# Optimization experiments

Hardware: AMD Instinct MI355X
Metric: run time of the kernel (lower is better)

The kernel has to match this reference:

```python
import jax, jax.numpy as jnp
import numpy as np

B, H, W, C = 16, 64, 64, 256
C8 = C // 8

def setup_inputs() -> dict:
    key = jax.random.key(0)
    ks = jax.random.split(key, 8)
    return {
        "x": jax.random.normal(ks[0], (B, H, W, C), dtype=jnp.float32),
        "Wf": jax.random.normal(ks[1], (C, C8), dtype=jnp.float32) * 0.05,
        "Wg": jax.random.normal(ks[2], (C, C8), dtype=jnp.float32) * 0.05,
        "Wh": jax.random.normal(ks[3], (C, C), dtype=jnp.float32) * 0.05,
        "bf": jax.random.normal(ks[4], (C8,), dtype=jnp.float32) * 0.05,
        "bg": jax.random.normal(ks[5], (C8,), dtype=jnp.float32) * 0.05,
        "bh": jax.random.normal(ks[6], (C,), dtype=jnp.float32) * 0.05,
        "gamma": jax.random.normal(ks[7], (1,), dtype=jnp.float32) * 0.05,
    }

def reference(x, Wf, Wg, Wh, bf, bg, bh, gamma):
    # 1x1 convs == per-pixel channel matmuls (NHWC)
    f = jnp.einsum('bhwc,cd->bhwd', x, Wf) + bf  # [B,H,W,C/8]
    g = jnp.einsum('bhwc,cd->bhwd', x, Wg) + bg  # [B,H,W,C/8]
    h = jnp.einsum('bhwc,cd->bhwd', x, Wh) + bh  # [B,H,W,C]
    b = x.shape[0]
    # K.batch_flatten flattens all non-batch dims -> attention over BATCH dim
    gf = g.reshape(b, -1)                      # [B, HWC/8]
    ff = f.reshape(b, -1)                      # [B, HWC/8]
    hf = h.reshape(b, -1)                      # [B, HWC]
    s = gf @ ff.T                              # [B, B]
    beta = jax.nn.softmax(s, axis=-1)          # softmax over batch axis
    o = (beta @ hf).reshape(x.shape)           # [B,H,W,C]
    # activation=None -> linear; gamma-scaled residual
    return gamma * o + x
```

## Files before the change

### kernel.cpp

```cpp
#include <hip/hip_runtime.h>

typedef __attribute__((ext_vector_type(4))) float  f4;
typedef __attribute__((ext_vector_type(2))) float  f2;
typedef __attribute__((ext_vector_type(8))) short  short8;
typedef __attribute__((ext_vector_type(4))) float  f32x4;
typedef __attribute__((ext_vector_type(2))) unsigned int u32x2;

static __device__ __forceinline__ unsigned short f2bf(float f) {
    unsigned u = __builtin_bit_cast(unsigned, f);
    unsigned r = (u + 0x7FFFu + ((u >> 16) & 1u)) >> 16;
    return (unsigned short)r;
}
static __device__ __forceinline__ float bf2f(unsigned short h) {
    return __builtin_bit_cast(float, ((unsigned)h) << 16);
}

__global__ __launch_bounds__(256) void k_setup(const float* __restrict__ Wh,
                                               const float* __restrict__ bh,
                                               const float* __restrict__ Wf,
                                               const float* __restrict__ Wg,
                                               const float* __restrict__ gamma,
                                               unsigned short* __restrict__ WhT,
                                               float* __restrict__ gb,
                                               unsigned short* __restrict__ Wfg_hi,
                                               unsigned short* __restrict__ Wfg_lo) {
    __shared__ float T[8 * 260];
    const int t = threadIdx.x, b = blockIdx.x;
    const float g = gamma[0];
    if (b < 32) {
        const int c0 = b * 8;
        const int cr = t >> 5, q = t & 31;
        f4 v0 = *(const f4*)(Wh + (c0 + cr) * 256 + q * 8);
        f4 v1 = *(const f4*)(Wh + (c0 + cr) * 256 + q * 8 + 4);
        *(f4*)(T + cr * 260 + q * 8)     = v0;
        *(f4*)(T + cr * 260 + q * 8 + 4) = v1;
        __syncthreads();
        short8 o;
        #pragma unroll
        for (int j = 0; j < 8; ++j) o[j] = (short)f2bf(g * T[j * 260 + t]);
        *(short8*)(WhT + t * 256 + c0) = o;
    } else {
        gb[t] = g * bh[t];
        const int n = t >> 2, cq = t & 3;
        const float* Wsrc = (n < 32) ? Wf : Wg;
        const int nn = n & 31;
        #pragma unroll
        for (int c8 = 0; c8 < 8; ++c8) {
            short8 h8, l8;
            #pragma unroll
            for (int k = 0; k < 8; ++k) {
                const int c = cq * 64 + c8 * 8 + k;
                const float v = Wsrc[c * 32 + nn];
                const unsigned short h = f2bf(v);
                h8[k] = (short)h;
                l8[k] = (short)f2bf(v - bf2f(h));
            }
            *(short8*)(Wfg_hi + n * 256 + cq * 64 + c8 * 8) = h8;
            *(short8*)(Wfg_lo + n * 256 + cq * 64 + c8 * 8) = l8;
        }
    }
}

__global__ __launch_bounds__(256, 2) void ka(const float* __restrict__ x,
                                             const unsigned short* __restrict__ Wfg_hi,
                                             const unsigned short* __restrict__ Wfg_lo,
                                             const float* __restrict__ bfv,
                                             const float* __restrict__ bgv,
                                             float* __restrict__ s_part) {
    __shared__ __align__(16) unsigned char smem[65536];

    const int t = threadIdx.x, w = t >> 6, l = t & 63;
    const int p = blockIdx.x * 4 + w;

    f4 xr[16];
    #pragma unroll
    for (int j = 0; j < 16; ++j)
        xr[j] = *(const f4*)(x + (((j << 12) + p) << 8) + l * 4);
    #pragma unroll
    for (int j = 0; j < 16; ++j) {
        const int r = j * 4 + w;
        int bo = r * 512 + l * 8;
        bo ^= (r & 7) << 4;
        const unsigned short h0 = f2bf(xr[j][0]), h1 = f2bf(xr[j][1]);
        const unsigned short h2 = f2bf(xr[j][2]), h3 = f2bf(xr[j][3]);
        u32x2 ph, pl;
        ph[0] = ((unsigned)h1 << 16) | h0;
        ph[1] = ((unsigned)h3 << 16) | h2;
        const unsigned short e0 = f2bf(xr[j][0] - bf2f(h0));
        const unsigned short e1 = f2bf(xr[j][1] - bf2f(h1));
        const unsigned short e2 = f2bf(xr[j][2] - bf2f(h2));
        const unsigned short e3 = f2bf(xr[j][3] - bf2f(h3));
        pl[0] = ((unsigned)e1 << 16) | e0;
        pl[1] = ((unsigned)e3 << 16) | e2;
        *(u32x2*)(smem + bo)         = ph;
        *(u32x2*)(smem + 32768 + bo) = pl;
    }
    __syncthreads();

    const int lrow = l & 15;
    const int kfe  = (l >> 4) * 8;
    const int ncol = w * 16 + lrow;
    f32x4 acc[4];
    #pragma unroll
    for (int mt = 0; mt < 4; ++mt) acc[mt] = (f32x4){0.f, 0.f, 0.f, 0.f};

    #pragma unroll
    for (int k0 = 0; k0 < 256; k0 += 32) {
        const short8 bh_ = *(const short8*)(Wfg_hi + ncol * 256 + k0 + kfe);
        const short8 bl_ = *(const short8*)(Wfg_lo + ncol * 256 + k0 + kfe);
        short8 ah[4], al[4];
        #pragma unroll
        for (int mt = 0; mt < 4; ++mt) {
            const int row = mt * 16 + lrow;
            int bo = row * 512 + (k0 + kfe) * 2;
            bo ^= (row & 7) << 4;
            ah[mt] = *(const short8*)(smem + bo);
            al[mt] = *(const short8*)(smem + 32768 + bo);
        }
        #pragma unroll
        for (int mt = 0; mt < 4; ++mt) {
            acc[mt] = __builtin_amdgcn_mfma_f32_16x16x32_bf16(ah[mt], bh_, acc[mt], 0, 0, 0);
            acc[mt] = __builtin_amdgcn_mfma_f32_16x16x32_bf16(al[mt], bh_, acc[mt], 0, 0, 0);
            acc[mt] = __builtin_amdgcn_mfma_f32_16x16x32_bf16(ah[mt], bl_, acc[mt], 0, 0, 0);
        }
    }
    __syncthreads();

    float* FG = (float*)smem;
    const float bias = (ncol < 32) ? bfv[ncol] : bgv[ncol - 32];
    #pragma unroll
    for (int mt = 0; mt < 4; ++mt)
        #pragma unroll
        for (int jj = 0; jj < 4; ++jj) {
            const int row = mt * 16 + (l >> 4) * 4 + jj;
            FG[row * 68 + ncol] = acc[mt][jj] + bias;
        }
    __syncthreads();

    const int si = t >> 4, sj = t & 15;
    float sacc = 0.f;
    #pragma unroll
    for (int q = 0; q < 4; ++q) {
        const float* Gp = FG + (si * 4 + q) * 68 + 32;
        const float* Fp = FG + (sj * 4 + q) * 68;
        #pragma unroll
        for (int d4 = 0; d4 < 8; ++d4) {
            f4 gv = *(const f4*)(Gp + d4 * 4);
            f4 fv = *(const f4*)(Fp + d4 * 4);
            sacc += gv[0] * fv[0] + gv[1] * fv[1] + gv[2] * fv[2] + gv[3] * fv[3];
        }
    }
    s_part[blockIdx.x * 256 + si * 16 + sj] = sacc;
}

__global__ __launch_bounds__(256) void kb1(const float* __restrict__ s_part,
                                           float* __restrict__ s_red) {
    const int t = threadIdx.x, b = blockIdx.x;
    float a = 0.f;
    #pragma unroll
    for (int k = 0; k < 16; ++k) a += s_part[(b * 16 + k) * 256 + t];
    s_red[b * 256 + t] = a;
}

__global__ __launch_bounds__(1024) void kb2(const float* __restrict__ s_red,
                                            float* __restrict__ beta) {
    __shared__ float red[4 * 256];
    __shared__ float srow[256];
    __shared__ float erow[256];
    const int t = threadIdx.x;
    const int pair = t & 255;
    const int qr = t >> 8;
    float a = 0.f;
    #pragma unroll
    for (int b = qr * 16; b < qr * 16 + 16; ++b) a += s_red[b * 256 + pair];
    red[qr * 256 + pair] = a;
    __syncthreads();
    float s = 0.f, e = 0.f;
    if (t < 256) {
        s = red[pair] + red[256 + pair] + red[512 + pair] + red[768 + pair];
        srow[pair] = s;
    }
    __syncthreads();
    if (t < 256) {
        const int i = pair >> 4;
        float m = srow[i * 16];
        #pragma unroll
        for (int j = 1; j < 16; ++j) m = fmaxf(m, srow[i * 16 + j]);
        e = expf(s - m);
        erow[pair] = e;
    }
    __syncthreads();
    if (t < 256) {
        const int i = pair >> 4;
        float sum = 0.f;
        #pragma unroll
        for (int j = 0; j < 16; ++j) sum += erow[i * 16 + j];
        beta[pair] = e / sum;
    }
}

__global__ __launch_bounds__(256, 3) void kc(const float* __restrict__ x,
                                             const unsigned short* __restrict__ WhT,
                                             const float* __restrict__ gb,
                                             const float* __restrict__ beta,
                                             float* __restrict__ out) {
    __shared__ __align__(16) unsigned char smem[34048];
    float* beta_l = (float*)(smem + 33024);

    const int t = threadIdx.x;
    const int w = t >> 6;
    const int l = t & 63;
    const int p0 = blockIdx.x * 4;
    const int p  = p0 + w;
    const int cbase = l * 4;

    f4 xr[16];
    #pragma unroll
    for (int j = 0; j < 16; ++j)
        xr[j] = *(const f4*)(x + (((j << 12) + p) << 8) + cbase);
    if (t < 64) *(f4*)(beta_l + t * 4) = *(const f4*)(beta + t * 4);
    __syncthreads();

    #pragma unroll
    for (int i = 0; i < 16; ++i) {
        f4 bv0 = *(const f4*)(beta_l + i * 16);
        f4 bv1 = *(const f4*)(beta_l + i * 16 + 4);
        f4 bv2 = *(const f4*)(beta_l + i * 16 + 8);
        f4 bv3 = *(const f4*)(beta_l + i * 16 + 12);
        f4 a = {0.f, 0.f, 0.f, 0.f};
        #pragma unroll
        for (int j = 0; j < 4; ++j) {
            a += xr[j]      * bv0[j];
            a += xr[4 + j]  * bv1[j];
            a += xr[8 + j]  * bv2[j];
            a += xr[12 + j] * bv3[j];
        }
        const int r = i * 4 + w;
        int bo = r * 512 + l * 8;
        bo ^= (r & 7) << 4;
        u32x2 packed;
        packed[0] = ((unsigned)f2bf(a[1]) << 16) | f2bf(a[0]);
        packed[1] = ((unsigned)f2bf(a[3]) << 16) | f2bf(a[2]);
        *(u32x2*)(smem + bo) = packed;
    }
    __syncthreads();

    f32x4 acc[4][4];
    #pragma unroll
    for (int mt = 0; mt < 4; ++mt)
        #pragma unroll
        for (int nt = 0; nt < 4; ++nt) acc[mt][nt] = (f32x4){0.f, 0.f, 0.f, 0.f};

    const int n0 = w * 64;
    const int lrow = l & 15;
    const int hi = l >> 4;
    const int kf = hi * 8;
    const unsigned short* wbase = WhT + (n0 + lrow) * 256 + kf;

    short8 bcur[4], bnxt[4];
    #pragma unroll
    for (int nt = 0; nt < 4; ++nt)
        bcur[nt] = *(const short8*)(wbase + nt * 16 * 256);

    #pragma unroll
    for (int ks = 0; ks < 8; ++ks) {
        const int k0 = ks * 32;
        if (ks < 7) {
            #pragma unroll
            for (int nt = 0; nt < 4; ++nt)
                bnxt[nt] = *(const short8*)(wbase + nt * 16 * 256 + k0 + 32);
        }
        short8 af[4];
        #pragma unroll
        for (int mt = 0; mt < 4; ++mt) {
            const int row = mt * 16 + lrow;
            int bo = row * 512 + (k0 + kf) * 2;
            bo ^= (row & 7) << 4;
            af[mt] = *(const short8*)(smem + bo);
        }
        #pragma unroll
        for (int mt = 0; mt < 4; ++mt)
            #pragma unroll
            for (int nt = 0; nt < 4; ++nt)
                acc[mt][nt] = __builtin_amdgcn_mfma_f32_16x16x32_bf16(
                    af[mt], bcur[nt], acc[mt][nt], 0, 0, 0);
        #pragma unroll
        for (int nt = 0; nt < 4; ++nt) bcur[nt] = bnxt[nt];
    }

    float* cst = (float*)smem;
    const f4 gb4 = *(const f4*)(gb + cbase);
    #pragma unroll
    for (int h = 0; h < 2; ++h) {
        __syncthreads();
        #pragma unroll
        for (int mt2 = 0; mt2 < 2; ++mt2) {
            const int mt = h * 2 + mt2;
            #pragma unroll
            for (int nt = 0; nt < 4; ++nt)
                #pragma unroll
                for (int j = 0; j < 4; ++j) {
                    const int rl = mt2 * 16 + hi * 4 + j;
                    cst[rl * 258 + n0 + nt * 16 + lrow] = acc[mt][nt][j];
                }
        }
        __syncthreads();
        #pragma unroll
        for (int rr = 0; rr < 8; ++rr) {
            const int rl = rr * 4 + w;
            const int rg = h * 32 + rl;
            const int i  = rg >> 2, q = rg & 3;
            const int idx = (((i << 12) + p0 + q) << 8) + cbase;
            f4 o = *(const f4*)(cst + rl * 258 + cbase);
            o += gb4 + *(const f4*)(x + idx);
            __builtin_nontemporal_store(o, (f4*)(out + idx));
        }
    }
}

extern "C" void kernel_launch(void* const* d_in, const int* in_sizes, int n_in,
                              void* d_out, int out_size, void* d_ws, size_t ws_size,
                              hipStream_t stream) {
    const float* x     = (const float*)d_in[0];
    const float* Wf    = (const float*)d_in[1];
    const float* Wg    = (const float*)d_in[2];
    const float* Wh    = (const float*)d_in[3];
    const float* bfv   = (const float*)d_in[4];
    const float* bgv   = (const float*)d_in[5];
    const float* bhv   = (const float*)d_in[6];
    const float* gamma = (const float*)d_in[7];
    float* out = (float*)d_out;

    char* ws = (char*)d_ws;
    unsigned short* WhT = (unsigned short*)ws;
    float* gb     = (float*)(ws + 131072);
    float* beta   = (float*)(ws + 132096);
    float* s_part = (float*)(ws + 133120);
    unsigned short* Wfg_hi = (unsigned short*)(ws + 1181696);
    unsigned short* Wfg_lo = (unsigned short*)(ws + 1214464);
    float* s_red  = (float*)(ws + 1181696);

    k_setup<<<dim3(33), dim3(256), 0, stream>>>(Wh, bhv, Wf, Wg, gamma, WhT, gb, Wfg_hi, Wfg_lo);
    ka<<<dim3(1024), dim3(256), 0, stream>>>(x, Wfg_hi, Wfg_lo, bfv, bgv, s_part);
    kb1<<<dim3(64), dim3(256), 0, stream>>>(s_part, s_red);
    kb2<<<dim3(1), dim3(1024), 0, stream>>>(s_red, beta);
    kc<<<dim3(1024), dim3(256), 0, stream>>>(x, WhT, gb, beta, out);
}
```

Before: 79.81 us.

## Process two pixel groups per block in kc, prefetching second x tile

Each kc block now handles two groups of four pixels instead of one, and the grid is halved. The second group's x rows are loaded into registers while the first group is being mixed and multiplied, so global load latency overlaps with MFMA and epilogue work. The staging and output shared-memory buffers are split so the second mix does not have to wait for the first epilogue's buffer. The cost is much higher register and LDS use, with launch bounds lowered to 2 blocks per CU, which reduces occupancy.

Result: no change. 80.07 us (+0.3%).

```diff
diff --git a/kernel.cpp b/kernel.cpp
--- a/kernel.cpp
+++ b/kernel.cpp
@@ -199,28 +199,8 @@
     }
 }
 
-__global__ __launch_bounds__(256, 3) void kc(const float* __restrict__ x,
-                                             const unsigned short* __restrict__ WhT,
-                                             const float* __restrict__ gb,
-                                             const float* __restrict__ beta,
-                                             float* __restrict__ out) {
-    __shared__ __align__(16) unsigned char smem[34048];
-    float* beta_l = (float*)(smem + 33024);
-
-    const int t = threadIdx.x;
-    const int w = t >> 6;
-    const int l = t & 63;
-    const int p0 = blockIdx.x * 4;
-    const int p  = p0 + w;
-    const int cbase = l * 4;
-
-    f4 xr[16];
-    #pragma unroll
-    for (int j = 0; j < 16; ++j)
-        xr[j] = *(const f4*)(x + (((j << 12) + p) << 8) + cbase);
-    if (t < 64) *(f4*)(beta_l + t * 4) = *(const f4*)(beta + t * 4);
-    __syncthreads();
-
+__device__ __forceinline__ void kc_mix(const f4 (&xr)[16], const float* beta_l,
+                                       unsigned char* stage, int w, int l) {
     #pragma unroll
     for (int i = 0; i < 16; ++i) {
         f4 bv0 = *(const f4*)(beta_l + i * 16);
@@ -241,21 +221,16 @@
         u32x2 packed;
         packed[0] = ((unsigned)f2bf(a[1]) << 16) | f2bf(a[0]);
         packed[1] = ((unsigned)f2bf(a[3]) << 16) | f2bf(a[2]);
-        *(u32x2*)(smem + bo) = packed;
-    }
-    __syncthreads();
-
-    f32x4 acc[4][4];
+        *(u32x2*)(stage + bo) = packed;
+    }
+}
+
+__device__ __forceinline__ void kc_gemm(f32x4 (&acc)[4][4], const unsigned char* stage,
+                                        const unsigned short* wbase, int lrow, int kf) {
     #pragma unroll
     for (int mt = 0; mt < 4; ++mt)
         #pragma unroll
         for (int nt = 0; nt < 4; ++nt) acc[mt][nt] = (f32x4){0.f, 0.f, 0.f, 0.f};
-
-    const int n0 = w * 64;
-    const int lrow = l & 15;
-    const int hi = l >> 4;
-    const int kf = hi * 8;
-    const unsigned short* wbase = WhT + (n0 + lrow) * 256 + kf;
 
     short8 bcur[4], bnxt[4];
     #pragma unroll
@@ -276,7 +251,7 @@
             const int row = mt * 16 + lrow;
             int bo = row * 512 + (k0 + kf) * 2;
             bo ^= (row & 7) << 4;
-            af[mt] = *(const short8*)(smem + bo);
+            af[mt] = *(const short8*)(stage + bo);
         }
         #pragma unroll
         for (int mt = 0; mt < 4; ++mt)
@@ -287,9 +262,12 @@
         #pragma unroll
         for (int nt = 0; nt < 4; ++nt) bcur[nt] = bnxt[nt];
     }
-
-    float* cst = (float*)smem;
-    const f4 gb4 = *(const f4*)(gb + cbase);
+}
+
+__device__ __forceinline__ void kc_epi(const f32x4 (&acc)[4][4], float* cst,
+                                       const float* __restrict__ x, float* __restrict__ out,
+                                       f4 gb4, int p0, int w, int l,
+                                       int n0, int lrow, int hi, int cbase) {
     #pragma unroll
     for (int h = 0; h < 2; ++h) {
         __syncthreads();
@@ -316,6 +294,54 @@
             __builtin_nontemporal_store(o, (f4*)(out + idx));
         }
     }
+}
+
+__global__ __launch_bounds__(256, 2) void kc(const float* __restrict__ x,
+                                             const unsigned short* __restrict__ WhT,
+                                             const float* __restrict__ gb,
+                                             const float* __restrict__ beta,
+                                             float* __restrict__ out) {
+    __shared__ __align__(16) unsigned char smem[66816];
+    unsigned char* stage = smem;
+    float* cst    = (float*)(smem + 32768);
+    float* beta_l = (float*)(smem + 65792);
+
+    const int t = threadIdx.x;
+    const int w = t >> 6;
+    const int l = t & 63;
+    const int p0A = blockIdx.x * 8;
+    const int p0B = p0A + 4;
+    const int pA = p0A + w;
+    const int pB = p0B + w;
+    const int cbase = l * 4;
+    const int n0 = w * 64;
+    const int lrow = l & 15;
+    const int hi = l >> 4;
+    const int kf = hi * 8;
+    const unsigned short* wbase = WhT + (n0 + lrow) * 256 + kf;
+    const f4 gb4 = *(const f4*)(gb + cbase);
+
+    f4 xrA[16], xrB[16];
+    #pragma unroll
+    for (int j = 0; j < 16; ++j)
+        xrA[j] = *(const f4*)(x + (((j << 12) + pA) << 8) + cbase);
+    if (t < 64) *(f4*)(beta_l + t * 4) = *(const f4*)(beta + t * 4);
+    __syncthreads();
+
+    kc_mix(xrA, beta_l, stage, w, l);
+    #pragma unroll
+    for (int j = 0; j < 16; ++j)
+        xrB[j] = *(const f4*)(x + (((j << 12) + pB) << 8) + cbase);
+    __syncthreads();
+
+    f32x4 acc[4][4];
+    kc_gemm(acc, stage, wbase, lrow, kf);
+    kc_epi(acc, cst, x, out, gb4, p0A, w, l, n0, lrow, hi, cbase);
+
+    kc_mix(xrB, beta_l, stage, w, l);
+    __syncthreads();
+    kc_gemm(acc, stage, wbase, lrow, kf);
+    kc_epi(acc, cst, x, out, gb4, p0B, w, l, n0, lrow, hi, cbase);
 }
 
 extern "C" void kernel_launch(void* const* d_in, const int* in_sizes, int n_in,
@@ -344,5 +370,5 @@
     ka<<<dim3(1024), dim3(256), 0, stream>>>(x, Wfg_hi, Wfg_lo, bfv, bgv, s_part);
     kb1<<<dim3(64), dim3(256), 0, stream>>>(s_part, s_red);
     kb2<<<dim3(1), dim3(1024), 0, stream>>>(s_red, beta);
-    kc<<<dim3(1024), dim3(256), 0, stream>>>(x, WhT, gb, beta, out);
-}
+    kc<<<dim3(512), dim3(256), 0, stream>>>(x, WhT, gb, beta, out);
+}
```

## Restructure output-projection kernel to one wave per pixel without block barriers

Applied to the files above, without the earlier changes.

The final beta-mix plus Wh projection kernel now runs one 64-thread wave per pixel instead of four waves sharing a 64-row tile. Each wave computes its own 16×256 MFMA output over the full N dimension, with a rolling two-deep prefetch of WhT fragments. The epilogue goes through a smaller XOR-swizzled LDS buffer. This drops all __syncthreads and shrinks LDS use per block to raise occupancy, but every wave now streams the whole WhT matrix. That quadruples L2 read traffic for the weights and reduces reuse per fetched B fragment.

Result: slower. 124.9 us (+56.5%).

```diff
diff --git a/kernel.cpp b/kernel.cpp
--- a/kernel.cpp
+++ b/kernel.cpp
@@ -199,27 +199,26 @@
     }
 }
 
-__global__ __launch_bounds__(256, 3) void kc(const float* __restrict__ x,
-                                             const unsigned short* __restrict__ WhT,
-                                             const float* __restrict__ gb,
-                                             const float* __restrict__ beta,
-                                             float* __restrict__ out) {
-    __shared__ __align__(16) unsigned char smem[34048];
-    float* beta_l = (float*)(smem + 33024);
-
-    const int t = threadIdx.x;
-    const int w = t >> 6;
-    const int l = t & 63;
-    const int p0 = blockIdx.x * 4;
-    const int p  = p0 + w;
+__global__ __launch_bounds__(64, 4) void kc(const float* __restrict__ x,
+                                            const unsigned short* __restrict__ WhT,
+                                            const float* __restrict__ gb,
+                                            const float* __restrict__ beta,
+                                            float* __restrict__ out) {
+    __shared__ __align__(16) unsigned char smem[9216];
+    float* beta_l = (float*)(smem + 8192);
+
+    const int l = threadIdx.x;
+    const int p = blockIdx.x;
     const int cbase = l * 4;
+    const int lrow = l & 15;
+    const int hi   = l >> 4;
+
+    *(f4*)(beta_l + l * 4) = *(const f4*)(beta + l * 4);
 
     f4 xr[16];
     #pragma unroll
     for (int j = 0; j < 16; ++j)
         xr[j] = *(const f4*)(x + (((j << 12) + p) << 8) + cbase);
-    if (t < 64) *(f4*)(beta_l + t * 4) = *(const f4*)(beta + t * 4);
-    __syncthreads();
 
     #pragma unroll
     for (int i = 0; i < 16; ++i) {
@@ -235,84 +234,66 @@
             a += xr[8 + j]  * bv2[j];
             a += xr[12 + j] * bv3[j];
         }
-        const int r = i * 4 + w;
-        int bo = r * 512 + l * 8;
-        bo ^= (r & 7) << 4;
+        int bo = i * 512 + l * 8;
+        bo ^= (i & 7) << 4;
         u32x2 packed;
         packed[0] = ((unsigned)f2bf(a[1]) << 16) | f2bf(a[0]);
         packed[1] = ((unsigned)f2bf(a[3]) << 16) | f2bf(a[2]);
         *(u32x2*)(smem + bo) = packed;
     }
-    __syncthreads();
-
-    f32x4 acc[4][4];
-    #pragma unroll
-    for (int mt = 0; mt < 4; ++mt)
-        #pragma unroll
-        for (int nt = 0; nt < 4; ++nt) acc[mt][nt] = (f32x4){0.f, 0.f, 0.f, 0.f};
-
-    const int n0 = w * 64;
-    const int lrow = l & 15;
-    const int hi = l >> 4;
-    const int kf = hi * 8;
-    const unsigned short* wbase = WhT + (n0 + lrow) * 256 + kf;
-
-    short8 bcur[4], bnxt[4];
-    #pragma unroll
-    for (int nt = 0; nt < 4; ++nt)
-        bcur[nt] = *(const short8*)(wbase + nt * 16 * 256);
-
-    #pragma unroll
-    for (int ks = 0; ks < 8; ++ks) {
-        const int k0 = ks * 32;
-        if (ks < 7) {
+
+    f32x4 acc[16];
+    #pragma unroll
+    for (int nt = 0; nt < 16; ++nt) acc[nt] = (f32x4){0.f, 0.f, 0.f, 0.f};
+
+    #pragma unroll
+    for (int kh = 0; kh < 2; ++kh) {
+        short8 af[4];
+        #pragma unroll
+        for (int ks = 0; ks < 4; ++ks) {
+            const int kb = kh * 128 + ks * 32;
+            int bo = lrow * 512 + (kb + hi * 8) * 2;
+            bo ^= (lrow & 7) << 4;
+            af[ks] = *(const short8*)(smem + bo);
+        }
+        const unsigned short* wb = WhT + lrow * 256 + kh * 128 + hi * 8;
+        short8 bpre[2];
+        bpre[0] = *(const short8*)(wb);
+        bpre[1] = *(const short8*)(wb + 32);
+        #pragma unroll
+        for (int q = 0; q < 64; ++q) {
+            short8 bc = bpre[q & 1];
+            if (q + 2 < 64) {
+                const int qn = q + 2;
+                bpre[q & 1] = *(const short8*)(wb + (qn >> 2) * (16 * 256) + (qn & 3) * 32);
+            }
+            acc[q >> 2] = __builtin_amdgcn_mfma_f32_16x16x32_bf16(
+                af[q & 3], bc, acc[q >> 2], 0, 0, 0);
+        }
+    }
+
+    #pragma unroll
+    for (int h = 0; h < 2; ++h) {
+        #pragma unroll
+        for (int nt2 = 0; nt2 < 8; ++nt2) {
+            const int nt = h * 8 + nt2;
             #pragma unroll
-            for (int nt = 0; nt < 4; ++nt)
-                bnxt[nt] = *(const short8*)(wbase + nt * 16 * 256 + k0 + 32);
-        }
-        short8 af[4];
-        #pragma unroll
-        for (int mt = 0; mt < 4; ++mt) {
-            const int row = mt * 16 + lrow;
-            int bo = row * 512 + (k0 + kf) * 2;
-            bo ^= (row & 7) << 4;
-            af[mt] = *(const short8*)(smem + bo);
-        }
-        #pragma unroll
-        for (int mt = 0; mt < 4; ++mt)
-            #pragma unroll
-            for (int nt = 0; nt < 4; ++nt)
-                acc[mt][nt] = __builtin_amdgcn_mfma_f32_16x16x32_bf16(
-                    af[mt], bcur[nt], acc[mt][nt], 0, 0, 0);
-        #pragma unroll
-        for (int nt = 0; nt < 4; ++nt) bcur[nt] = bnxt[nt];
-    }
-
-    float* cst = (float*)smem;
-    const f4 gb4 = *(const f4*)(gb + cbase);
-    #pragma unroll
-    for (int h = 0; h < 2; ++h) {
-        __syncthreads();
-        #pragma unroll
-        for (int mt2 = 0; mt2 < 2; ++mt2) {
-            const int mt = h * 2 + mt2;
-            #pragma unroll
-            for (int nt = 0; nt < 4; ++nt)
-                #pragma unroll
-                for (int j = 0; j < 4; ++j) {
-                    const int rl = mt2 * 16 + hi * 4 + j;
-                    cst[rl * 258 + n0 + nt * 16 + lrow] = acc[mt][nt][j];
-                }
-        }
-        __syncthreads();
+            for (int j = 0; j < 4; ++j) {
+                const int i = hi * 4 + j;
+                int ad = i * 512 + (nt2 * 16 + lrow) * 4;
+                ad ^= (i & 7) << 4;
+                *(float*)(smem + ad) = acc[nt][j];
+            }
+        }
         #pragma unroll
         for (int rr = 0; rr < 8; ++rr) {
-            const int rl = rr * 4 + w;
-            const int rg = h * 32 + rl;
-            const int i  = rg >> 2, q = rg & 3;
-            const int idx = (((i << 12) + p0 + q) << 8) + cbase;
-            f4 o = *(const f4*)(cst + rl * 258 + cbase);
-            o += gb4 + *(const f4*)(x + idx);
+            const int i = rr * 2 + (l >> 5);
+            int ad = i * 512 + (l & 31) * 16;
+            ad ^= (i & 7) << 4;
+            f4 o = *(const f4*)(smem + ad);
+            const int c = h * 128 + (l & 31) * 4;
+            const int idx = (((i << 12) + p) << 8) + c;
+            o += *(const f4*)(gb + c) + *(const f4*)(x + idx);
             __builtin_nontemporal_store(o, (f4*)(out + idx));
         }
     }
@@ -344,5 +325,5 @@
     ka<<<dim3(1024), dim3(256), 0, stream>>>(x, Wfg_hi, Wfg_lo, bfv, bgv, s_part);
     kb1<<<dim3(64), dim3(256), 0, stream>>>(s_part, s_red);
     kb2<<<dim3(1), dim3(1024), 0, stream>>>(s_red, beta);
-    kc<<<dim3(1024), dim3(256), 0, stream>>>(x, WhT, gb, beta, out);
-}
+    kc<<<dim3(4096), dim3(64), 0, stream>>>(x, WhT, gb, beta, out);
+}
```

## Split batch-mix and Wh GEMM into two kernels via workspace bf16 image

Applied to the files above, without the earlier changes.

The fused final kernel is split in two. The first kernel mixes x across the batch with beta and writes a pre-swizzled bf16 tile image to workspace. The second kernel loads that image into LDS and runs the MFMA GEMM plus the residual epilogue, with the x residual loads issued before the barrier. The aim is to raise occupancy (launch bounds 4 instead of 3) and shorten the per-kernel dependency chain, at the cost of an extra 32 MB write and read of the intermediate and one more launch. A fallback keeps the fused kernel when the workspace is too small.

Measured after the change: 99.18 us. +24.3%, slower.

```diff
diff --git a/kernel.cpp b/kernel.cpp
--- a/kernel.cpp
+++ b/kernel.cpp
@@ -199,11 +199,164 @@
     }
 }
 
-__global__ __launch_bounds__(256, 3) void kc(const float* __restrict__ x,
-                                             const unsigned short* __restrict__ WhT,
-                                             const float* __restrict__ gb,
-                                             const float* __restrict__ beta,
-                                             float* __restrict__ out) {
+__device__ __forceinline__ void kc_mix(const f4 (&xr)[16], const float* beta_l,
+                                       unsigned char* stage, int w, int l) {
+    #pragma unroll
+    for (int i = 0; i < 16; ++i) {
+        f4 bv0 = *(const f4*)(beta_l + i * 16);
+        f4 bv1 = *(const f4*)(beta_l + i * 16 + 4);
+        f4 bv2 = *(const f4*)(beta_l + i * 16 + 8);
+        f4 bv3 = *(const f4*)(beta_l + i * 16 + 12);
+        f4 a = {0.f, 0.f, 0.f, 0.f};
+        #pragma unroll
+        for (int j = 0; j < 4; ++j) {
+            a += xr[j]      * bv0[j];
+            a += xr[4 + j]  * bv1[j];
+            a += xr[8 + j]  * bv2[j];
+            a += xr[12 + j] * bv3[j];
+        }
+        const int r = i * 4 + w;
+        int bo = r * 512 + l * 8;
+        bo ^= (r & 7) << 4;
+        u32x2 packed;
+        packed[0] = ((unsigned)f2bf(a[1]) << 16) | f2bf(a[0]);
+        packed[1] = ((unsigned)f2bf(a[3]) << 16) | f2bf(a[2]);
+        *(u32x2*)(stage + bo) = packed;
+    }
+}
+
+__device__ __forceinline__ void kc_gemm(f32x4 (&acc)[4][4], const unsigned char* stage,
+                                        const unsigned short* wbase, int lrow, int kf) {
+    #pragma unroll
+    for (int mt = 0; mt < 4; ++mt)
+        #pragma unroll
+        for (int nt = 0; nt < 4; ++nt) acc[mt][nt] = (f32x4){0.f, 0.f, 0.f, 0.f};
+
+    short8 bcur[4], bnxt[4];
+    #pragma unroll
+    for (int nt = 0; nt < 4; ++nt)
+        bcur[nt] = *(const short8*)(wbase + nt * 16 * 256);
+
+    #pragma unroll
+    for (int ks = 0; ks < 8; ++ks) {
+        const int k0 = ks * 32;
+        if (ks < 7) {
+            #pragma unroll
+            for (int nt = 0; nt < 4; ++nt)
+                bnxt[nt] = *(const short8*)(wbase + nt * 16 * 256 + k0 + 32);
+        }
+        short8 af[4];
+        #pragma unroll
+        for (int mt = 0; mt < 4; ++mt) {
+            const int row = mt * 16 + lrow;
+            int bo = row * 512 + (k0 + kf) * 2;
+            bo ^= (row & 7) << 4;
+            af[mt] = *(const short8*)(stage + bo);
+        }
+        #pragma unroll
+        for (int mt = 0; mt < 4; ++mt)
+            #pragma unroll
+            for (int nt = 0; nt < 4; ++nt)
+                acc[mt][nt] = __builtin_amdgcn_mfma_f32_16x16x32_bf16(
+                    af[mt], bcur[nt], acc[mt][nt], 0, 0, 0);
+        #pragma unroll
+        for (int nt = 0; nt < 4; ++nt) bcur[nt] = bnxt[nt];
+    }
+}
+
+__global__ __launch_bounds__(256, 4) void kc1(const float* __restrict__ x,
+                                              const float* __restrict__ beta,
+                                              unsigned char* __restrict__ xmimg) {
+    __shared__ float beta_l[256];
+    const int t = threadIdx.x, w = t >> 6, l = t & 63;
+    const int p = blockIdx.x * 4 + w;
+    const int cbase = l * 4;
+
+    f4 xr[16];
+    #pragma unroll
+    for (int j = 0; j < 16; ++j)
+        xr[j] = *(const f4*)(x + (((j << 12) + p) << 8) + cbase);
+    if (t < 64) *(f4*)(beta_l + t * 4) = *(const f4*)(beta + t * 4);
+    __syncthreads();
+
+    kc_mix(xr, beta_l, xmimg + (size_t)blockIdx.x * 32768, w, l);
+}
+
+__global__ __launch_bounds__(256, 4) void kc2(const float* __restrict__ x,
+                                              const unsigned short* __restrict__ WhT,
+                                              const float* __restrict__ gb,
+                                              const unsigned char* __restrict__ xmimg,
+                                              float* __restrict__ out) {
+    __shared__ __align__(16) unsigned char smem[33024];
+
+    const int t = threadIdx.x;
+    const int w = t >> 6;
+    const int l = t & 63;
+    const int p0 = blockIdx.x * 4;
+    const int cbase = l * 4;
+    const int n0 = w * 64;
+    const int lrow = l & 15;
+    const int hi = l >> 4;
+    const int kf = hi * 8;
+    const unsigned short* wbase = WhT + (n0 + lrow) * 256 + kf;
+
+    {
+        const unsigned char* img = xmimg + (size_t)blockIdx.x * 32768;
+        f4 v[8];
+        #pragma unroll
+        for (int k = 0; k < 8; ++k)
+            v[k] = *(const f4*)(img + (k * 256 + t) * 16);
+        #pragma unroll
+        for (int k = 0; k < 8; ++k)
+            *(f4*)(smem + (k * 256 + t) * 16) = v[k];
+    }
+    __syncthreads();
+
+    f32x4 acc[4][4];
+    kc_gemm(acc, smem, wbase, lrow, kf);
+
+    float* cst = (float*)smem;
+    const f4 gb4 = *(const f4*)(gb + cbase);
+    #pragma unroll
+    for (int h = 0; h < 2; ++h) {
+        f4 xa[8];
+        #pragma unroll
+        for (int rr = 0; rr < 8; ++rr) {
+            const int rg = h * 32 + rr * 4 + w;
+            const int i  = rg >> 2, q = rg & 3;
+            xa[rr] = *(const f4*)(x + (((i << 12) + p0 + q) << 8) + cbase);
+        }
+        __syncthreads();
+        #pragma unroll
+        for (int mt2 = 0; mt2 < 2; ++mt2) {
+            const int mt = h * 2 + mt2;
+            #pragma unroll
+            for (int nt = 0; nt < 4; ++nt)
+                #pragma unroll
+                for (int j = 0; j < 4; ++j) {
+                    const int rl = mt2 * 16 + hi * 4 + j;
+                    cst[rl * 258 + n0 + nt * 16 + lrow] = acc[mt][nt][j];
+                }
+        }
+        __syncthreads();
+        #pragma unroll
+        for (int rr = 0; rr < 8; ++rr) {
+            const int rl = rr * 4 + w;
+            const int rg = h * 32 + rl;
+            const int i  = rg >> 2, q = rg & 3;
+            const int idx = (((i << 12) + p0 + q) << 8) + cbase;
+            f4 o = *(const f4*)(cst + rl * 258 + cbase);
+            o += gb4 + xa[rr];
+            __builtin_nontemporal_store(o, (f4*)(out + idx));
+        }
+    }
+}
+
+__global__ __launch_bounds__(256, 3) void kc_fused(const float* __restrict__ x,
+                                                   const unsigned short* __restrict__ WhT,
+                                                   const float* __restrict__ gb,
+                                                   const float* __restrict__ beta,
+                                                   float* __restrict__ out) {
     __shared__ __align__(16) unsigned char smem[34048];
     float* beta_l = (float*)(smem + 33024);
 
@@ -213,80 +366,24 @@
     const int p0 = blockIdx.x * 4;
     const int p  = p0 + w;
     const int cbase = l * 4;
-
-    f4 xr[16];
-    #pragma unroll
-    for (int j = 0; j < 16; ++j)
-        xr[j] = *(const f4*)(x + (((j << 12) + p) << 8) + cbase);
-    if (t < 64) *(f4*)(beta_l + t * 4) = *(const f4*)(beta + t * 4);
-    __syncthreads();
-
-    #pragma unroll
-    for (int i = 0; i < 16; ++i) {
-        f4 bv0 = *(const f4*)(beta_l + i * 16);
-        f4 bv1 = *(const f4*)(beta_l + i * 16 + 4);
-        f4 bv2 = *(const f4*)(beta_l + i * 16 + 8);
-        f4 bv3 = *(const f4*)(beta_l + i * 16 + 12);
-        f4 a = {0.f, 0.f, 0.f, 0.f};
-        #pragma unroll
-        for (int j = 0; j < 4; ++j) {
-            a += xr[j]      * bv0[j];
-            a += xr[4 + j]  * bv1[j];
-            a += xr[8 + j]  * bv2[j];
-            a += xr[12 + j] * bv3[j];
-        }
-        const int r = i * 4 + w;
-        int bo = r * 512 + l * 8;
-        bo ^= (r & 7) << 4;
-        u32x2 packed;
-        packed[0] = ((unsigned)f2bf(a[1]) << 16) | f2bf(a[0]);
-        packed[1] = ((unsigned)f2bf(a[3]) << 16) | f2bf(a[2]);
-        *(u32x2*)(smem + bo) = packed;
-    }
-    __syncthreads();
-
-    f32x4 acc[4][4];
-    #pragma unroll
-    for (int mt = 0; mt < 4; ++mt)
-        #pragma unroll
-        for (int nt = 0; nt < 4; ++nt) acc[mt][nt] = (f32x4){0.f, 0.f, 0.f, 0.f};
-
     const int n0 = w * 64;
     const int lrow = l & 15;
     const int hi = l >> 4;
     const int kf = hi * 8;
     const unsigned short* wbase = WhT + (n0 + lrow) * 256 + kf;
 
-    short8 bcur[4], bnxt[4];
-    #pragma unroll
-    for (int nt = 0; nt < 4; ++nt)
-        bcur[nt] = *(const short8*)(wbase + nt * 16 * 256);
-
-    #pragma unroll
-    for (int ks = 0; ks < 8; ++ks) {
-        const int k0 = ks * 32;
-        if (ks < 7) {
-            #pragma unroll
-            for (int nt = 0; nt < 4; ++nt)
-                bnxt[nt] = *(const short8*)(wbase + nt * 16 * 256 + k0 + 32);
-        }
-        short8 af[4];
-        #pragma unroll
-        for (int mt = 0; mt < 4; ++mt) {
-            const int row = mt * 16 + lrow;
-            int bo = row * 512 + (k0 + kf) * 2;
-            bo ^= (row & 7) << 4;
-            af[mt] = *(const short8*)(smem + bo);
-        }
-        #pragma unroll
-        for (int mt = 0; mt < 4; ++mt)
-            #pragma unroll
-            for (int nt = 0; nt < 4; ++nt)
-                acc[mt][nt] = __builtin_amdgcn_mfma_f32_16x16x32_bf16(
-                    af[mt], bcur[nt], acc[mt][nt], 0, 0, 0);
-        #pragma unroll
-        for (int nt = 0; nt < 4; ++nt) bcur[nt] = bnxt[nt];
-    }
+    f4 xr[16];
+    #pragma unroll
+    for (int j = 0; j < 16; ++j)
+        xr[j] = *(const f4*)(x + (((j << 12) + p) << 8) + cbase);
+    if (t < 64) *(f4*)(beta_l + t * 4) = *(const f4*)(beta + t * 4);
+    __syncthreads();
+
+    kc_mix(xr, beta_l, smem, w, l);
+    __syncthreads();
+
+    f32x4 acc[4][4];
+    kc_gemm(acc, smem, wbase, lrow, kf);
 
     float* cst = (float*)smem;
     const f4 gb4 = *(const f4*)(gb + cbase);
@@ -339,10 +436,17 @@
     unsigned short* Wfg_hi = (unsigned short*)(ws + 1181696);
     unsigned short* Wfg_lo = (unsigned short*)(ws + 1214464);
     float* s_red  = (float*)(ws + 1181696);
+    unsigned char* xmimg = (unsigned char*)(ws + 2097152);
 
     k_setup<<<dim3(33), dim3(256), 0, stream>>>(Wh, bhv, Wf, Wg, gamma, WhT, gb, Wfg_hi, Wfg_lo);
     ka<<<dim3(1024), dim3(256), 0, stream>>>(x, Wfg_hi, Wfg_lo, bfv, bgv, s_part);
     kb1<<<dim3(64), dim3(256), 0, stream>>>(s_part, s_red);
     kb2<<<dim3(1), dim3(1024), 0, stream>>>(s_red, beta);
-    kc<<<dim3(1024), dim3(256), 0, stream>>>(x, WhT, gb, beta, out);
-}
+
+    if (ws_size >= 2097152ull + 33554432ull) {
+        kc1<<<dim3(1024), dim3(256), 0, stream>>>(x, beta, xmimg);
+        kc2<<<dim3(1024), dim3(256), 0, stream>>>(x, WhT, gb, xmimg, out);
+    } else {
+        kc_fused<<<dim3(1024), dim3(256), 0, stream>>>(x, WhT, gb, beta, out);
+    }
+}
```
